# Kernel optimization log

Measured on AMD Instinct MI355X. Metric: run time of the kernel, lower is better.

Reference implementation:

```python
import jax, jax.numpy as jnp
import numpy as np

EPS = 1e-5
POOL = 4  # two stacked AvgPool3d(2) == one AvgPool3d(4, stride=4) on the valid region


def setup_inputs() -> dict:
    key = jax.random.key(0)
    k1, k2, k3 = jax.random.split(key, 3)
    N, Cin, Cout, D = 16, 32, 16, 32
    x = jax.random.normal(k1, (N, Cin, D, D, D), dtype=jnp.float32)
    w = jax.random.normal(k2, (Cin, Cout, 3, 3, 3), dtype=jnp.float32) * 0.1
    b = jax.random.normal(k3, (Cout,), dtype=jnp.float32) * 0.1
    gamma = jnp.ones((Cout,), dtype=jnp.float32)
    beta = jnp.zeros((Cout,), dtype=jnp.float32)
    return {"x": x, "w": w, "b": b, "gamma": gamma, "beta": beta}


def _convT_bn_pool(x, w, b, gamma, beta):
    # ConvTranspose3d(stride=2, padding=1, K=3) == dilated conv with
    # lhs_dilation=2, padding=K-1-p=1, spatially-flipped kernel, IO->OI swap.
    wt = jnp.flip(w, axis=(2, 3, 4)).transpose(1, 0, 2, 3, 4)  # [Cout,Cin,3,3,3]
    y = jax.lax.conv_general_dilated(
        x, wt,
        window_strides=(1, 1, 1),
        padding=[(1, 1), (1, 1), (1, 1)],
        lhs_dilation=(2, 2, 2),
        dimension_numbers=("NCDHW", "OIDHW", "NCDHW"),
    )
    y = y + b[None, :, None, None, None]  # [N,Cout,Dout,Hout,Wout], Dout=2D-1

    # BatchNorm training stats: biased variance over (N,D,H,W) per channel
    mean = jnp.mean(y, axis=(0, 2, 3, 4), keepdims=True)
    var = jnp.mean(jnp.square(y - mean), axis=(0, 2, 3, 4), keepdims=True)
    inv = jax.lax.rsqrt(var + EPS)
    yn = (y - mean) * inv * gamma[None, :, None, None, None] + beta[None, :, None, None, None]

    # Two AvgPool3d(2) == AvgPool3d(4, stride 4) on the cropped valid region
    N_, C_, Do, Ho, Wo = yn.shape
    D2, H2, W2 = Do // POOL, Ho // POOL, Wo // POOL
    yn = yn[:, :, : D2 * POOL, : H2 * POOL, : W2 * POOL]
    yn = yn.reshape(N_, C_, D2, POOL, H2, POOL, W2, POOL)
    return jnp.mean(yn, axis=(3, 5, 7))  # [N,C,D2,H2,W2]


def reference(x, w, b, gamma, beta):
    return _convT_bn_pool(x, w, b, gamma, beta)
```

## Files before the change

kernel.cpp:

```cpp
#include <hip/hip_runtime.h>


typedef __attribute__((ext_vector_type(8))) short bf16x8;
typedef __attribute__((ext_vector_type(4))) float f32x4;

static __device__ __forceinline__ unsigned short f2bf(float f) {
    unsigned int u = __float_as_uint(f);
    u = (u + 0x7fffu + ((u >> 16) & 1u)) >> 16;
    return (unsigned short)u;
}
static __device__ __forceinline__ unsigned cvtpk(float a, float b) {
    unsigned r;
    asm("v_cvt_pk_bf16_f32 %0, %1, %2" : "=v"(r) : "v"(a), "v"(b));
    return r;
}

__global__ __launch_bounds__(256)
void kw(const float* __restrict__ w, unsigned short* __restrict__ wT)
{
    const int idx = blockIdx.x * 256 + threadIdx.x;
    if (idx < 13824) {
        const int ci = idx & 31, co = (idx >> 5) & 15, tap = idx >> 9;
        wT[idx] = f2bf(w[(ci * 16 + co) * 27 + tap]);
    }
}

__global__ __launch_bounds__(256, 4)
void convf2(const float* __restrict__ x,
            const unsigned short* __restrict__ wT,
            const float* __restrict__ bias,
            float* __restrict__ pooled,
            float* __restrict__ psum, float* __restrict__ psq)
{
    const int ht = blockIdx.x, dt = blockIdx.y, n = blockIdx.z;
    const int tid = threadIdx.x;
    const int v = tid >> 6, lane = tid & 63;
    const int t = v & 1, odp = v >> 1;
    const int c = lane & 15, qd = lane >> 4;

    __shared__ alignas(16) unsigned short xs[9504];
    __shared__ alignas(16) unsigned short wTs[13824];
    __shared__ float sred[4][16], qred[4][16], pbuf[2][8][16];

    const float bv = bias[c];

    #pragma unroll
    for (int i = 0; i < 7; ++i) {
        const int chunk = v + 4 * i;
        if (chunk < 27) {
            __builtin_amdgcn_global_load_lds(
                (const char*)wT + chunk * 1024 + lane * 16,
                (char*)wTs + chunk * 1024,
                16, 0, 0);
        }
    }

    const int ciS = tid >> 3, q = tid & 7;
    const int oL = ciS & 7;
    const float* xbase = x + (n*32 + ciS)*32768 + 4*q;
    float4 F[9];
    #pragma unroll
    for (int p = 0; p < 9; ++p) {
        const int di = p / 3, hi = p - 3*(p/3);
        const int id = 2*dt + di, ih = 2*ht + hi;
        const bool ok = (id < 32) && (ih < 32);
        F[p] = ok ? *(const float4*)(xbase + id*1024 + ih*32)
                  : make_float4(0.f, 0.f, 0.f, 0.f);
    }

    const unsigned selP = (lane & 8) ? 0x07060302u : 0x01000504u;
    const int iwT = 4*q + (oL & 3), hT = oL >> 2;
    #pragma unroll
    for (int p = 0; p < 9; ++p) {
        unsigned u0 = cvtpk(F[p].x, F[p].y);
        unsigned u1 = cvtpk(F[p].z, F[p].w);
        const unsigned a0 = (unsigned)__shfl_xor((int)u0, 8, 64);
        const unsigned a1 = (unsigned)__shfl_xor((int)u1, 8, 64);
        u0 = __builtin_amdgcn_perm(u0, a0, selP);
        u1 = __builtin_amdgcn_perm(u1, a1, selP);
        const unsigned t0 = (unsigned)__shfl_xor((int)u0, 16, 64);
        const unsigned t1 = (unsigned)__shfl_xor((int)u1, 16, 64);
        const unsigned n0 = (lane & 16) ? t1 : u0;
        const unsigned n1 = (lane & 16) ? u1 : t0;
        *(uint2*)(xs + p*1056 + v*264 + iwT*8 + 4*hT) = make_uint2(n0, n1);
    }
    if (tid < 36) {
        const int dihi = tid >> 2, gg = tid & 3;
        *(uint4*)(xs + dihi*1056 + gg*264 + 256) = make_uint4(0,0,0,0);
    }

    __syncthreads();

    f32x4 acc[2][4][2];
    #pragma unroll
    for (int ol = 0; ol < 2; ++ol)
        #pragma unroll
        for (int oh = 0; oh < 4; ++oh)
            #pragma unroll
            for (int par = 0; par < 2; ++par)
                acc[ol][oh][par] = (f32x4){0.f,0.f,0.f,0.f};

    const int iwb = 16 * t + c;
    auto LDA = [&](int dihi, int sofs) -> bf16x8 {
        return *(const bf16x8*)(xs + dihi*1056 + qd*264 + (iwb + sofs)*8);
    };
    auto LDB = [&](int tap) -> bf16x8 {
        return *(const bf16x8*)(wTs + tap*512 + c*32 + qd*8);
    };

    constexpr int KHP[3][2][2] = {
        {{1,1},{2,3}},
        {{0,0},{1,2}},
        {{0,1},{1,3}},
    };
    const int PB[3]  = {9, 18, 0};
    const int POL[3] = {0, 1, 1};
    const int PDI[3] = {odp, odp, odp + 1};

    bf16x8 B0 = LDB(9 + 0), B1 = LDB(9 + 1), B2 = LDB(9 + 2);
    #pragma unroll
    for (int s = 0; s < 9; ++s) {
        const int ph = s / 3;
        bf16x8 N0, N1, N2;
        if (s < 8) {
            const int sn = s + 1;
            const int phn = sn / 3, khn = sn - 3*(sn/3);
            const int bn_ = PB[phn] + khn * 3;
            N0 = LDB(bn_ + 0); N1 = LDB(bn_ + 1); N2 = LDB(bn_ + 2);
        }
        const int kh = s - 3*(s/3);
        const int ol = POL[ph], di = PDI[ph];
        #pragma unroll
        for (int pp = 0; pp < 2; ++pp) {
            const int hi = KHP[kh][pp][0], oh = KHP[kh][pp][1];
            const bf16x8 A0 = LDA(di*3 + hi, 0), A1 = LDA(di*3 + hi, 1);
            acc[ol][oh][0] = __builtin_amdgcn_mfma_f32_16x16x32_bf16(
                A0, B1, acc[ol][oh][0], 0, 0, 0);
            acc[ol][oh][1] = __builtin_amdgcn_mfma_f32_16x16x32_bf16(
                A1, B0, acc[ol][oh][1], 0, 0, 0);
            acc[ol][oh][1] = __builtin_amdgcn_mfma_f32_16x16x32_bf16(
                A0, B2, acc[ol][oh][1], 0, 0, 0);
        }
        if (s < 8) { B0 = N0; B1 = N1; B2 = N2; }
    }

    float s = 0.f, sq = 0.f;
    float P[2] = {0.f, 0.f};
    #pragma unroll
    for (int ol = 0; ol < 2; ++ol) {
        const int odg = 2*odp + ol;
        const bool odok = !(dt == 15 && odg == 3);
        #pragma unroll
        for (int oh = 0; oh < 4; ++oh) {
            const bool ohok = !(ht == 15 && oh == 3);
            #pragma unroll
            for (int par = 0; par < 2; ++par)
                #pragma unroll
                for (int r = 0; r < 4; ++r) {
                    const float val = acc[ol][oh][par][r] + bv;
                    const bool owok = !(par == 1 && t == 1 && qd == 3 && r == 3);
                    const float mk = (odok && ohok && owok) ? 1.f : 0.f;
                    s += mk * val; sq += mk * val * val;
                    P[r >> 1] += val;
                }
        }
    }
    s  += __shfl_xor(s, 16, 64);  s  += __shfl_xor(s, 32, 64);
    sq += __shfl_xor(sq, 16, 64); sq += __shfl_xor(sq, 32, 64);

    if (lane < 16) { sred[v][lane] = s; qred[v][lane] = sq; }
    if (odp == 0 && dt < 15 && ht < 15) {
        pbuf[t][2*qd + 0][c] = P[0];
        pbuf[t][2*qd + 1][c] = P[1];
    }
    __syncthreads();
    if (tid < 16) {
        const int blk = (n*16 + dt)*16 + ht;
        psum[tid*4096 + blk] = sred[0][tid]+sred[1][tid]+sred[2][tid]+sred[3][tid];
        psq [tid*4096 + blk] = qred[0][tid]+qred[1][tid]+qred[2][tid]+qred[3][tid];
    }
    if (odp == 1 && dt < 15 && ht < 15) {
        #pragma unroll
        for (int jj = 0; jj < 2; ++jj) {
            const int jl = 2*qd + jj, jg = 8*t + jl;
            if (jg < 15) {
                const float tot = pbuf[t][jl][c] + P[jj];
                pooled[(n*16 + c)*3375 + dt*225 + ht*15 + jg] = tot * (1.f/64.f);
            }
        }
    }
}

__global__ void bnfinal(const float* __restrict__ psum, const float* __restrict__ psq,
                        const float* __restrict__ gamma, const float* __restrict__ beta,
                        float* __restrict__ bn)
{
    const int co = blockIdx.x;
    const int t  = threadIdx.x;
    float S = 0, Q = 0;
    for (int blk = t; blk < 4096; blk += 256) {
        S += psum[co*4096 + blk];
        Q += psq [co*4096 + blk];
    }
    #pragma unroll
    for (int off = 32; off > 0; off >>= 1) {
        S += __shfl_down(S, off, 64);
        Q += __shfl_down(Q, off, 64);
    }
    __shared__ float rs[4], rq[4];
    if ((t & 63) == 0) { rs[t >> 6] = S; rq[t >> 6] = Q; }
    __syncthreads();
    if (t == 0) {
        S = rs[0] + rs[1] + rs[2] + rs[3];
        Q = rq[0] + rq[1] + rq[2] + rq[3];
        const float cnt = 16.f * 63.f * 63.f * 63.f;
        const float mean = S / cnt;
        const float var  = Q / cnt - mean * mean;
        const float inv  = rsqrtf(var + 1e-5f);
        const float sc   = inv * gamma[co];
        bn[co]      = sc;
        bn[16 + co] = beta[co] - mean * sc;
    }
}

__global__ void finalize(const float* __restrict__ pooled, const float* __restrict__ bn,
                         float* __restrict__ out)
{
    const int i  = blockIdx.x * 256 + threadIdx.x;
    const int co = (i / 3375) & 15;
    out[i] = pooled[i] * bn[co] + bn[16 + co];
}

extern "C" void kernel_launch(void* const* d_in, const int* in_sizes, int n_in,
                              void* d_out, int out_size, void* d_ws, size_t ws_size,
                              hipStream_t stream)
{
    const float* x     = (const float*)d_in[0];
    const float* w     = (const float*)d_in[1];
    const float* b     = (const float*)d_in[2];
    const float* gamma = (const float*)d_in[3];
    const float* beta  = (const float*)d_in[4];
    float* out = (float*)d_out;

    char* wsb = (char*)d_ws;
    unsigned short* wT = (unsigned short*)wsb;
    float* pooled = (float*)(wsb + 27648);
    float* psum   = (float*)(wsb + 27648 + 3456000);
    float* psq    = (float*)(wsb + 27648 + 3456000 + 262144);
    float* bn     = (float*)(wsb + 27648 + 3456000 + 2*262144);

    kw<<<54, 256, 0, stream>>>(w, wT);
    dim3 grid(16, 16, 16);
    convf2<<<grid, 256, 0, stream>>>(x, wT, b, pooled, psum, psq);
    bnfinal<<<16, 256, 0, stream>>>(psum, psq, gamma, beta, bn);
    finalize<<<3375, 256, 0, stream>>>(pooled, bn, out);
}
```

Before: 131.9 us.

## Process four batch items per conv block with double-buffered input prefetch

```diff
diff --git a/kernel.cpp b/kernel.cpp
--- a/kernel.cpp
+++ b/kernel.cpp
@@ -25,22 +25,23 @@
     }
 }
 
-__global__ __launch_bounds__(256, 4)
+__global__ __launch_bounds__(256, 2)
 void convf2(const float* __restrict__ x,
             const unsigned short* __restrict__ wT,
             const float* __restrict__ bias,
             float* __restrict__ pooled,
             float* __restrict__ psum, float* __restrict__ psq)
 {
-    const int ht = blockIdx.x, dt = blockIdx.y, n = blockIdx.z;
+    const int ht = blockIdx.x, dt = blockIdx.y, bz = blockIdx.z;
+    const int n0 = bz * 4;
     const int tid = threadIdx.x;
     const int v = tid >> 6, lane = tid & 63;
-    const int t = v & 1, odp = v >> 1;
+    const int tw = v & 1, odp = v >> 1;
     const int c = lane & 15, qd = lane >> 4;
 
-    __shared__ alignas(16) unsigned short xs[9504];
+    __shared__ alignas(16) unsigned short xs[2][9504];
     __shared__ alignas(16) unsigned short wTs[13824];
-    __shared__ float sred[4][16], qred[4][16], pbuf[2][8][16];
+    __shared__ float sred[4][16], qred[4][16], pbuf[2][2][8][16];
 
     const float bv = bias[c];
 
@@ -57,56 +58,50 @@
 
     const int ciS = tid >> 3, q = tid & 7;
     const int oL = ciS & 7;
-    const float* xbase = x + (n*32 + ciS)*32768 + 4*q;
-    float4 F[9];
+    int  offp[9]; bool okp[9];
     #pragma unroll
     for (int p = 0; p < 9; ++p) {
         const int di = p / 3, hi = p - 3*(p/3);
         const int id = 2*dt + di, ih = 2*ht + hi;
-        const bool ok = (id < 32) && (ih < 32);
-        F[p] = ok ? *(const float4*)(xbase + id*1024 + ih*32)
-                  : make_float4(0.f, 0.f, 0.f, 0.f);
-    }
-
+        okp[p]  = (id < 32) && (ih < 32);
+        offp[p] = id*1024 + ih*32;
+    }
+    float4 F[9];
+    auto ISSUE = [&](int nn) {
+        const float* xb = x + (size_t)(nn*32 + ciS)*32768 + 4*q;
+        #pragma unroll
+        for (int p = 0; p < 9; ++p)
+            F[p] = okp[p] ? *(const float4*)(xb + offp[p])
+                          : make_float4(0.f, 0.f, 0.f, 0.f);
+    };
     const unsigned selP = (lane & 8) ? 0x07060302u : 0x01000504u;
     const int iwT = 4*q + (oL & 3), hT = oL >> 2;
-    #pragma unroll
-    for (int p = 0; p < 9; ++p) {
-        unsigned u0 = cvtpk(F[p].x, F[p].y);
-        unsigned u1 = cvtpk(F[p].z, F[p].w);
-        const unsigned a0 = (unsigned)__shfl_xor((int)u0, 8, 64);
-        const unsigned a1 = (unsigned)__shfl_xor((int)u1, 8, 64);
-        u0 = __builtin_amdgcn_perm(u0, a0, selP);
-        u1 = __builtin_amdgcn_perm(u1, a1, selP);
-        const unsigned t0 = (unsigned)__shfl_xor((int)u0, 16, 64);
-        const unsigned t1 = (unsigned)__shfl_xor((int)u1, 16, 64);
-        const unsigned n0 = (lane & 16) ? t1 : u0;
-        const unsigned n1 = (lane & 16) ? u1 : t0;
-        *(uint2*)(xs + p*1056 + v*264 + iwT*8 + 4*hT) = make_uint2(n0, n1);
-    }
+    auto TRANSP = [&](int buf) {
+        unsigned short* xp = &xs[buf][0];
+        #pragma unroll
+        for (int p = 0; p < 9; ++p) {
+            unsigned u0 = cvtpk(F[p].x, F[p].y);
+            unsigned u1 = cvtpk(F[p].z, F[p].w);
+            const unsigned a0 = (unsigned)__shfl_xor((int)u0, 8, 64);
+            const unsigned a1 = (unsigned)__shfl_xor((int)u1, 8, 64);
+            u0 = __builtin_amdgcn_perm(u0, a0, selP);
+            u1 = __builtin_amdgcn_perm(u1, a1, selP);
+            const unsigned b0 = (unsigned)__shfl_xor((int)u0, 16, 64);
+            const unsigned b1 = (unsigned)__shfl_xor((int)u1, 16, 64);
+            const unsigned w0 = (lane & 16) ? b1 : u0;
+            const unsigned w1 = (lane & 16) ? u1 : b0;
+            *(uint2*)(xp + p*1056 + v*264 + iwT*8 + 4*hT) = make_uint2(w0, w1);
+        }
+    };
+
+    ISSUE(n0);
     if (tid < 36) {
         const int dihi = tid >> 2, gg = tid & 3;
-        *(uint4*)(xs + dihi*1056 + gg*264 + 256) = make_uint4(0,0,0,0);
-    }
-
+        *(uint4*)(&xs[0][0] + dihi*1056 + gg*264 + 256) = make_uint4(0,0,0,0);
+        *(uint4*)(&xs[1][0] + dihi*1056 + gg*264 + 256) = make_uint4(0,0,0,0);
+    }
+    TRANSP(0);
     __syncthreads();
-
-    f32x4 acc[2][4][2];
-    #pragma unroll
-    for (int ol = 0; ol < 2; ++ol)
-        #pragma unroll
-        for (int oh = 0; oh < 4; ++oh)
-            #pragma unroll
-            for (int par = 0; par < 2; ++par)
-                acc[ol][oh][par] = (f32x4){0.f,0.f,0.f,0.f};
-
-    const int iwb = 16 * t + c;
-    auto LDA = [&](int dihi, int sofs) -> bf16x8 {
-        return *(const bf16x8*)(xs + dihi*1056 + qd*264 + (iwb + sofs)*8);
-    };
-    auto LDB = [&](int tap) -> bf16x8 {
-        return *(const bf16x8*)(wTs + tap*512 + c*32 + qd*8);
-    };
 
     constexpr int KHP[3][2][2] = {
         {{1,1},{2,3}},
@@ -116,78 +111,116 @@
     const int PB[3]  = {9, 18, 0};
     const int POL[3] = {0, 1, 1};
     const int PDI[3] = {odp, odp, odp + 1};
-
-    bf16x8 B0 = LDB(9 + 0), B1 = LDB(9 + 1), B2 = LDB(9 + 2);
-    #pragma unroll
-    for (int s = 0; s < 9; ++s) {
-        const int ph = s / 3;
-        bf16x8 N0, N1, N2;
-        if (s < 8) {
-            const int sn = s + 1;
-            const int phn = sn / 3, khn = sn - 3*(sn/3);
-            const int bn_ = PB[phn] + khn * 3;
-            N0 = LDB(bn_ + 0); N1 = LDB(bn_ + 1); N2 = LDB(bn_ + 2);
-        }
-        const int kh = s - 3*(s/3);
-        const int ol = POL[ph], di = PDI[ph];
-        #pragma unroll
-        for (int pp = 0; pp < 2; ++pp) {
-            const int hi = KHP[kh][pp][0], oh = KHP[kh][pp][1];
-            const bf16x8 A0 = LDA(di*3 + hi, 0), A1 = LDA(di*3 + hi, 1);
-            acc[ol][oh][0] = __builtin_amdgcn_mfma_f32_16x16x32_bf16(
-                A0, B1, acc[ol][oh][0], 0, 0, 0);
-            acc[ol][oh][1] = __builtin_amdgcn_mfma_f32_16x16x32_bf16(
-                A1, B0, acc[ol][oh][1], 0, 0, 0);
-            acc[ol][oh][1] = __builtin_amdgcn_mfma_f32_16x16x32_bf16(
-                A0, B2, acc[ol][oh][1], 0, 0, 0);
-        }
-        if (s < 8) { B0 = N0; B1 = N1; B2 = N2; }
-    }
-
-    float s = 0.f, sq = 0.f;
-    float P[2] = {0.f, 0.f};
-    #pragma unroll
-    for (int ol = 0; ol < 2; ++ol) {
-        const int odg = 2*odp + ol;
-        const bool odok = !(dt == 15 && odg == 3);
-        #pragma unroll
-        for (int oh = 0; oh < 4; ++oh) {
-            const bool ohok = !(ht == 15 && oh == 3);
-            #pragma unroll
-            for (int par = 0; par < 2; ++par)
+    const int iwb = 16 * tw + c;
+    auto LDB = [&](int tap) -> bf16x8 {
+        return *(const bf16x8*)(wTs + tap*512 + c*32 + qd*8);
+    };
+    const bool pok = (dt < 15) && (ht < 15);
+
+    float sA = 0.f, sqA = 0.f;
+    float Pd[2] = {0.f, 0.f};
+
+    auto POOLW = [&](int t) {
+        if (odp == 1 && pok) {
+            #pragma unroll
+            for (int jj = 0; jj < 2; ++jj) {
+                const int jl = 2*qd + jj, jg = 8*tw + jl;
+                if (jg < 15) {
+                    const float tot = pbuf[t & 1][tw][jl][c] + Pd[jj];
+                    pooled[((n0 + t)*16 + c)*3375 + dt*225 + ht*15 + jg]
+                        = tot * (1.f/64.f);
+                }
+            }
+        }
+    };
+
+    for (int tt = 0; tt < 4; ++tt) {
+        const int cur = tt & 1;
+        if (tt < 3) ISSUE(n0 + tt + 1);
+        if (tt > 0) POOLW(tt - 1);
+
+        const unsigned short* xcur = &xs[cur][0];
+        auto LDA = [&](int dihi, int sofs) -> bf16x8 {
+            return *(const bf16x8*)(xcur + dihi*1056 + qd*264 + (iwb + sofs)*8);
+        };
+
+        f32x4 acc[2][4][2];
+        #pragma unroll
+        for (int ol = 0; ol < 2; ++ol)
+            #pragma unroll
+            for (int oh = 0; oh < 4; ++oh)
                 #pragma unroll
-                for (int r = 0; r < 4; ++r) {
-                    const float val = acc[ol][oh][par][r] + bv;
-                    const bool owok = !(par == 1 && t == 1 && qd == 3 && r == 3);
-                    const float mk = (odok && ohok && owok) ? 1.f : 0.f;
-                    s += mk * val; sq += mk * val * val;
-                    P[r >> 1] += val;
-                }
-        }
-    }
-    s  += __shfl_xor(s, 16, 64);  s  += __shfl_xor(s, 32, 64);
-    sq += __shfl_xor(sq, 16, 64); sq += __shfl_xor(sq, 32, 64);
-
-    if (lane < 16) { sred[v][lane] = s; qred[v][lane] = sq; }
-    if (odp == 0 && dt < 15 && ht < 15) {
-        pbuf[t][2*qd + 0][c] = P[0];
-        pbuf[t][2*qd + 1][c] = P[1];
-    }
+                for (int par = 0; par < 2; ++par)
+                    acc[ol][oh][par] = (f32x4){0.f,0.f,0.f,0.f};
+
+        bf16x8 B0 = LDB(9 + 0), B1 = LDB(9 + 1), B2 = LDB(9 + 2);
+        #pragma unroll
+        for (int s = 0; s < 9; ++s) {
+            const int ph = s / 3;
+            bf16x8 N0, N1, N2;
+            if (s < 8) {
+                const int sn = s + 1;
+                const int phn = sn / 3, khn = sn - 3*(sn/3);
+                const int bn_ = PB[phn] + khn * 3;
+                N0 = LDB(bn_ + 0); N1 = LDB(bn_ + 1); N2 = LDB(bn_ + 2);
+            }
+            const int kh = s - 3*(s/3);
+            const int ol = POL[ph], di = PDI[ph];
+            #pragma unroll
+            for (int pp = 0; pp < 2; ++pp) {
+                const int hi = KHP[kh][pp][0], oh = KHP[kh][pp][1];
+                const bf16x8 A0 = LDA(di*3 + hi, 0), A1 = LDA(di*3 + hi, 1);
+                acc[ol][oh][0] = __builtin_amdgcn_mfma_f32_16x16x32_bf16(
+                    A0, B1, acc[ol][oh][0], 0, 0, 0);
+                acc[ol][oh][1] = __builtin_amdgcn_mfma_f32_16x16x32_bf16(
+                    A1, B0, acc[ol][oh][1], 0, 0, 0);
+                acc[ol][oh][1] = __builtin_amdgcn_mfma_f32_16x16x32_bf16(
+                    A0, B2, acc[ol][oh][1], 0, 0, 0);
+            }
+            if (s < 8) { B0 = N0; B1 = N1; B2 = N2; }
+        }
+
+        float P[2] = {0.f, 0.f};
+        #pragma unroll
+        for (int ol = 0; ol < 2; ++ol) {
+            const int odg = 2*odp + ol;
+            const bool odok = !(dt == 15 && odg == 3);
+            #pragma unroll
+            for (int oh = 0; oh < 4; ++oh) {
+                const bool ohok = !(ht == 15 && oh == 3);
+                #pragma unroll
+                for (int par = 0; par < 2; ++par)
+                    #pragma unroll
+                    for (int r = 0; r < 4; ++r) {
+                        const float val = acc[ol][oh][par][r] + bv;
+                        const bool owok = !(par == 1 && tw == 1 && qd == 3 && r == 3);
+                        const float mk = (odok && ohok && owok) ? 1.f : 0.f;
+                        sA += mk * val; sqA += mk * val * val;
+                        P[r >> 1] += val;
+                    }
+            }
+        }
+        if (odp == 0 && pok) {
+            pbuf[cur][tw][2*qd + 0][c] = P[0];
+            pbuf[cur][tw][2*qd + 1][c] = P[1];
+        } else {
+            Pd[0] = P[0]; Pd[1] = P[1];
+        }
+
+        if (tt < 3) TRANSP(cur ^ 1);
+        __syncthreads();
+    }
+
+    POOLW(3);
+
+    sA  += __shfl_xor(sA, 16, 64);  sA  += __shfl_xor(sA, 32, 64);
+    sqA += __shfl_xor(sqA, 16, 64); sqA += __shfl_xor(sqA, 32, 64);
+    if (lane < 16) { sred[v][lane] = sA; qred[v][lane] = sqA; }
     __syncthreads();
     if (tid < 16) {
-        const int blk = (n*16 + dt)*16 + ht;
+        const int blk = (bz*16 + dt)*16 + ht;
         psum[tid*4096 + blk] = sred[0][tid]+sred[1][tid]+sred[2][tid]+sred[3][tid];
         psq [tid*4096 + blk] = qred[0][tid]+qred[1][tid]+qred[2][tid]+qred[3][tid];
-    }
-    if (odp == 1 && dt < 15 && ht < 15) {
-        #pragma unroll
-        for (int jj = 0; jj < 2; ++jj) {
-            const int jl = 2*qd + jj, jg = 8*t + jl;
-            if (jg < 15) {
-                const float tot = pbuf[t][jl][c] + P[jj];
-                pooled[(n*16 + c)*3375 + dt*225 + ht*15 + jg] = tot * (1.f/64.f);
-            }
-        }
     }
 }
 
@@ -198,7 +231,7 @@
     const int co = blockIdx.x;
     const int t  = threadIdx.x;
     float S = 0, Q = 0;
-    for (int blk = t; blk < 4096; blk += 256) {
+    for (int blk = t; blk < 1024; blk += 256) {
         S += psum[co*4096 + blk];
         Q += psq [co*4096 + blk];
     }
@@ -250,7 +283,7 @@
     float* bn     = (float*)(wsb + 27648 + 3456000 + 2*262144);
 
     kw<<<54, 256, 0, stream>>>(w, wT);
-    dim3 grid(16, 16, 16);
+    dim3 grid(16, 16, 4);
     convf2<<<grid, 256, 0, stream>>>(x, wT, b, pooled, psum, psq);
     bnfinal<<<16, 256, 0, stream>>>(psum, psq, gamma, beta, bn);
     finalize<<<3375, 256, 0, stream>>>(pooled, bn, out);
```

Result: faster. 128.3 us (-2.7%).

## Split conv work across 8 waves per block instead of 4

Applied to the files above, without the earlier changes.

```diff
diff --git a/kernel.cpp b/kernel.cpp
--- a/kernel.cpp
+++ b/kernel.cpp
@@ -25,7 +25,7 @@
     }
 }
 
-__global__ __launch_bounds__(256, 4)
+__global__ __launch_bounds__(512, 4)
 void convf2(const float* __restrict__ x,
             const unsigned short* __restrict__ wT,
             const float* __restrict__ bias,
@@ -34,19 +34,19 @@
 {
     const int ht = blockIdx.x, dt = blockIdx.y, n = blockIdx.z;
     const int tid = threadIdx.x;
-    const int v = tid >> 6, lane = tid & 63;
-    const int t = v & 1, odp = v >> 1;
+    const int vv = tid >> 6, lane = tid & 63;
+    const int tw = vv & 1, odq = vv >> 1;
     const int c = lane & 15, qd = lane >> 4;
 
     __shared__ alignas(16) unsigned short xs[9504];
     __shared__ alignas(16) unsigned short wTs[13824];
-    __shared__ float sred[4][16], qred[4][16], pbuf[2][8][16];
+    __shared__ float sred[8][16], qred[8][16], pbuf[4][2][8][16];
 
     const float bv = bias[c];
 
     #pragma unroll
-    for (int i = 0; i < 7; ++i) {
-        const int chunk = v + 4 * i;
+    for (int i = 0; i < 4; ++i) {
+        const int chunk = vv + 8 * i;
         if (chunk < 27) {
             __builtin_amdgcn_global_load_lds(
                 (const char*)wT + chunk * 1024 + lane * 16,
@@ -55,34 +55,41 @@
         }
     }
 
-    const int ciS = tid >> 3, q = tid & 7;
+    const int h = tid >> 8, ltid = tid & 255;
+    const int ciS = ltid >> 3, q = ltid & 7;
     const int oL = ciS & 7;
-    const float* xbase = x + (n*32 + ciS)*32768 + 4*q;
-    float4 F[9];
-    #pragma unroll
-    for (int p = 0; p < 9; ++p) {
-        const int di = p / 3, hi = p - 3*(p/3);
-        const int id = 2*dt + di, ih = 2*ht + hi;
-        const bool ok = (id < 32) && (ih < 32);
-        F[p] = ok ? *(const float4*)(xbase + id*1024 + ih*32)
-                  : make_float4(0.f, 0.f, 0.f, 0.f);
-    }
-
+    const int g = ciS >> 3;
+    const float* xbase = x + (size_t)(n*32 + ciS)*32768 + 4*q;
+    float4 F[5];
+    #pragma unroll
+    for (int i = 0; i < 5; ++i) {
+        const int p = 2*i + h;
+        if (p < 9) {
+            const int di = p / 3, hp = p - 3*(p/3);
+            const int id = 2*dt + di, ih = 2*ht + hp;
+            F[i] = (id < 32 && ih < 32)
+                 ? *(const float4*)(xbase + id*1024 + ih*32)
+                 : make_float4(0.f, 0.f, 0.f, 0.f);
+        }
+    }
     const unsigned selP = (lane & 8) ? 0x07060302u : 0x01000504u;
     const int iwT = 4*q + (oL & 3), hT = oL >> 2;
     #pragma unroll
-    for (int p = 0; p < 9; ++p) {
-        unsigned u0 = cvtpk(F[p].x, F[p].y);
-        unsigned u1 = cvtpk(F[p].z, F[p].w);
-        const unsigned a0 = (unsigned)__shfl_xor((int)u0, 8, 64);
-        const unsigned a1 = (unsigned)__shfl_xor((int)u1, 8, 64);
-        u0 = __builtin_amdgcn_perm(u0, a0, selP);
-        u1 = __builtin_amdgcn_perm(u1, a1, selP);
-        const unsigned t0 = (unsigned)__shfl_xor((int)u0, 16, 64);
-        const unsigned t1 = (unsigned)__shfl_xor((int)u1, 16, 64);
-        const unsigned n0 = (lane & 16) ? t1 : u0;
-        const unsigned n1 = (lane & 16) ? u1 : t0;
-        *(uint2*)(xs + p*1056 + v*264 + iwT*8 + 4*hT) = make_uint2(n0, n1);
+    for (int i = 0; i < 5; ++i) {
+        const int p = 2*i + h;
+        if (p < 9) {
+            unsigned u0 = cvtpk(F[i].x, F[i].y);
+            unsigned u1 = cvtpk(F[i].z, F[i].w);
+            const unsigned a0 = (unsigned)__shfl_xor((int)u0, 8, 64);
+            const unsigned a1 = (unsigned)__shfl_xor((int)u1, 8, 64);
+            u0 = __builtin_amdgcn_perm(u0, a0, selP);
+            u1 = __builtin_amdgcn_perm(u1, a1, selP);
+            const unsigned s0 = (unsigned)__shfl_xor((int)u0, 16, 64);
+            const unsigned s1 = (unsigned)__shfl_xor((int)u1, 16, 64);
+            const unsigned w0 = (lane & 16) ? s1 : u0;
+            const unsigned w1 = (lane & 16) ? u1 : s0;
+            *(uint2*)(xs + p*1056 + g*264 + iwT*8 + 4*hT) = make_uint2(w0, w1);
+        }
     }
     if (tid < 36) {
         const int dihi = tid >> 2, gg = tid & 3;
@@ -91,100 +98,92 @@
 
     __syncthreads();
 
-    f32x4 acc[2][4][2];
-    #pragma unroll
-    for (int ol = 0; ol < 2; ++ol)
-        #pragma unroll
-        for (int oh = 0; oh < 4; ++oh)
-            #pragma unroll
-            for (int par = 0; par < 2; ++par)
-                acc[ol][oh][par] = (f32x4){0.f,0.f,0.f,0.f};
-
-    const int iwb = 16 * t + c;
+    f32x4 acc[4][2];
+    #pragma unroll
+    for (int oh = 0; oh < 4; ++oh)
+        #pragma unroll
+        for (int par = 0; par < 2; ++par)
+            acc[oh][par] = (f32x4){0.f,0.f,0.f,0.f};
+
+    const int iwb = 16 * tw + c;
     auto LDA = [&](int dihi, int sofs) -> bf16x8 {
         return *(const bf16x8*)(xs + dihi*1056 + qd*264 + (iwb + sofs)*8);
     };
     auto LDB = [&](int tap) -> bf16x8 {
         return *(const bf16x8*)(wTs + tap*512 + c*32 + qd*8);
     };
-
     constexpr int KHP[3][2][2] = {
         {{1,1},{2,3}},
         {{0,0},{1,2}},
         {{0,1},{1,3}},
     };
-    const int PB[3]  = {9, 18, 0};
-    const int POL[3] = {0, 1, 1};
-    const int PDI[3] = {odp, odp, odp + 1};
-
-    bf16x8 B0 = LDB(9 + 0), B1 = LDB(9 + 1), B2 = LDB(9 + 2);
-    #pragma unroll
-    for (int s = 0; s < 9; ++s) {
-        const int ph = s / 3;
-        bf16x8 N0, N1, N2;
-        if (s < 8) {
-            const int sn = s + 1;
-            const int phn = sn / 3, khn = sn - 3*(sn/3);
-            const int bn_ = PB[phn] + khn * 3;
-            N0 = LDB(bn_ + 0); N1 = LDB(bn_ + 1); N2 = LDB(bn_ + 2);
-        }
-        const int kh = s - 3*(s/3);
-        const int ol = POL[ph], di = PDI[ph];
-        #pragma unroll
-        for (int pp = 0; pp < 2; ++pp) {
-            const int hi = KHP[kh][pp][0], oh = KHP[kh][pp][1];
-            const bf16x8 A0 = LDA(di*3 + hi, 0), A1 = LDA(di*3 + hi, 1);
-            acc[ol][oh][0] = __builtin_amdgcn_mfma_f32_16x16x32_bf16(
-                A0, B1, acc[ol][oh][0], 0, 0, 0);
-            acc[ol][oh][1] = __builtin_amdgcn_mfma_f32_16x16x32_bf16(
-                A1, B0, acc[ol][oh][1], 0, 0, 0);
-            acc[ol][oh][1] = __builtin_amdgcn_mfma_f32_16x16x32_bf16(
-                A0, B2, acc[ol][oh][1], 0, 0, 0);
-        }
-        if (s < 8) { B0 = N0; B1 = N1; B2 = N2; }
-    }
-
-    float s = 0.f, sq = 0.f;
+    auto PH = [&](int base, int di) {
+        #pragma unroll
+        for (int kh = 0; kh < 3; ++kh) {
+            const bf16x8 B0 = LDB(base + kh*3 + 0);
+            const bf16x8 B1 = LDB(base + kh*3 + 1);
+            const bf16x8 B2 = LDB(base + kh*3 + 2);
+            #pragma unroll
+            for (int pp = 0; pp < 2; ++pp) {
+                const int hi = KHP[kh][pp][0], oh = KHP[kh][pp][1];
+                const bf16x8 A0 = LDA(di*3 + hi, 0), A1 = LDA(di*3 + hi, 1);
+                acc[oh][0] = __builtin_amdgcn_mfma_f32_16x16x32_bf16(
+                    A0, B1, acc[oh][0], 0, 0, 0);
+                acc[oh][1] = __builtin_amdgcn_mfma_f32_16x16x32_bf16(
+                    A1, B0, acc[oh][1], 0, 0, 0);
+                acc[oh][1] = __builtin_amdgcn_mfma_f32_16x16x32_bf16(
+                    A0, B2, acc[oh][1], 0, 0, 0);
+            }
+        }
+    };
+    const int m = odq >> 1;
+    if ((odq & 1) == 0) {
+        PH(9, m);
+    } else {
+        PH(18, m);
+        PH(0,  m + 1);
+    }
+
+    float sA = 0.f, sqA = 0.f;
     float P[2] = {0.f, 0.f};
-    #pragma unroll
-    for (int ol = 0; ol < 2; ++ol) {
-        const int odg = 2*odp + ol;
-        const bool odok = !(dt == 15 && odg == 3);
-        #pragma unroll
-        for (int oh = 0; oh < 4; ++oh) {
-            const bool ohok = !(ht == 15 && oh == 3);
+    const bool odok = !(dt == 15 && odq == 3);
+    #pragma unroll
+    for (int oh = 0; oh < 4; ++oh) {
+        const bool ohok = !(ht == 15 && oh == 3);
+        #pragma unroll
+        for (int par = 0; par < 2; ++par)
             #pragma unroll
-            for (int par = 0; par < 2; ++par)
-                #pragma unroll
-                for (int r = 0; r < 4; ++r) {
-                    const float val = acc[ol][oh][par][r] + bv;
-                    const bool owok = !(par == 1 && t == 1 && qd == 3 && r == 3);
-                    const float mk = (odok && ohok && owok) ? 1.f : 0.f;
-                    s += mk * val; sq += mk * val * val;
-                    P[r >> 1] += val;
-                }
-        }
-    }
-    s  += __shfl_xor(s, 16, 64);  s  += __shfl_xor(s, 32, 64);
-    sq += __shfl_xor(sq, 16, 64); sq += __shfl_xor(sq, 32, 64);
-
-    if (lane < 16) { sred[v][lane] = s; qred[v][lane] = sq; }
-    if (odp == 0 && dt < 15 && ht < 15) {
-        pbuf[t][2*qd + 0][c] = P[0];
-        pbuf[t][2*qd + 1][c] = P[1];
-    }
+            for (int r = 0; r < 4; ++r) {
+                const float val = acc[oh][par][r] + bv;
+                const bool owok = !(par == 1 && tw == 1 && qd == 3 && r == 3);
+                const float mk = (odok && ohok && owok) ? 1.f : 0.f;
+                sA += mk * val; sqA += mk * val * val;
+                P[r >> 1] += val;
+            }
+    }
+    sA  += __shfl_xor(sA, 16, 64);  sA  += __shfl_xor(sA, 32, 64);
+    sqA += __shfl_xor(sqA, 16, 64); sqA += __shfl_xor(sqA, 32, 64);
+    if (lane < 16) { sred[vv][lane] = sA; qred[vv][lane] = sqA; }
+    pbuf[odq][tw][2*qd + 0][c] = P[0];
+    pbuf[odq][tw][2*qd + 1][c] = P[1];
+
     __syncthreads();
+
     if (tid < 16) {
         const int blk = (n*16 + dt)*16 + ht;
-        psum[tid*4096 + blk] = sred[0][tid]+sred[1][tid]+sred[2][tid]+sred[3][tid];
-        psq [tid*4096 + blk] = qred[0][tid]+qred[1][tid]+qred[2][tid]+qred[3][tid];
-    }
-    if (odp == 1 && dt < 15 && ht < 15) {
+        float S = 0.f, Q = 0.f;
+        #pragma unroll
+        for (int wv = 0; wv < 8; ++wv) { S += sred[wv][tid]; Q += qred[wv][tid]; }
+        psum[tid*4096 + blk] = S;
+        psq [tid*4096 + blk] = Q;
+    }
+    if (odq == 3 && dt < 15 && ht < 15) {
         #pragma unroll
         for (int jj = 0; jj < 2; ++jj) {
-            const int jl = 2*qd + jj, jg = 8*t + jl;
+            const int jl = 2*qd + jj, jg = 8*tw + jl;
             if (jg < 15) {
-                const float tot = pbuf[t][jl][c] + P[jj];
+                const float tot = pbuf[0][tw][jl][c] + pbuf[1][tw][jl][c]
+                                + pbuf[2][tw][jl][c] + pbuf[3][tw][jl][c];
                 pooled[(n*16 + c)*3375 + dt*225 + ht*15 + jg] = tot * (1.f/64.f);
             }
         }
@@ -251,7 +250,7 @@
 
     kw<<<54, 256, 0, stream>>>(w, wT);
     dim3 grid(16, 16, 16);
-    convf2<<<grid, 256, 0, stream>>>(x, wT, b, pooled, psum, psq);
+    convf2<<<grid, 512, 0, stream>>>(x, wT, b, pooled, psum, psq);
     bnfinal<<<16, 256, 0, stream>>>(psum, psq, gamma, beta, bn);
     finalize<<<3375, 256, 0, stream>>>(pooled, bn, out);
 }
```

Result: slower. 134.6 us (+2.0%).
